# Performance work log

Hardware: AMD Instinct MI355X
Metric: run time of the kernel (lower is better)

## Reference

```python
import jax, jax.numpy as jnp
import numpy as np

DIM = 768
NUM_HEADS = 12
HEAD_DIM = DIM // NUM_HEADS
HW = 32  # input_size = (32, 32)


def setup_inputs() -> dict:
    key = jax.random.key(0)
    ks = jax.random.split(key, 7)
    return {
        "x": jax.random.normal(ks[0], (8, HW, HW, DIM), dtype=jnp.float32),
        "w_qkv": jax.random.normal(ks[1], (DIM, 3 * DIM), dtype=jnp.float32) * 0.02,
        "b_qkv": jnp.zeros((3 * DIM,), dtype=jnp.float32),
        "w_proj": jax.random.normal(ks[2], (DIM, DIM), dtype=jnp.float32) * 0.02,
        "b_proj": jnp.zeros((DIM,), dtype=jnp.float32),
        "rel_pos_h": jax.random.normal(ks[3], (2 * HW - 1, HEAD_DIM), dtype=jnp.float32) * 0.02,
        "rel_pos_w": jax.random.normal(ks[4], (2 * HW - 1, HEAD_DIM), dtype=jnp.float32) * 0.02,
    }


def _gather_rel_pos(size, rel_pos):
    # q_size == k_size == size, so no resize; index = i - j + (size - 1)
    idx = jnp.arange(size)[:, None] - jnp.arange(size)[None, :] + (size - 1)
    return rel_pos[idx]  # [size, size, head_dim]


def reference(x, w_qkv, b_qkv, w_proj, b_proj, rel_pos_h, rel_pos_w):
    B, H, W, C = x.shape
    nH, D = NUM_HEADS, HEAD_DIM
    scale = D ** -0.5
    S = H * W

    qkv = x.reshape(B, S, C) @ w_qkv + b_qkv          # [B,S,3C]
    qkv = qkv.reshape(B, S, 3, nH, D).transpose(2, 0, 3, 1, 4)  # [3,B,nH,S,D]
    q, k, v = qkv[0], qkv[1], qkv[2]

    attn = jnp.einsum('bnsd,bntd->bnst', q * scale, k)  # [B,nH,S,S]

    # decomposed relative positional bias
    Rh = _gather_rel_pos(H, rel_pos_h)                  # [H,H,D]
    Rw = _gather_rel_pos(W, rel_pos_w)                  # [W,W,D]
    r_q = q.reshape(B, nH, H, W, D)
    rel_h = jnp.einsum('bnhwc,hkc->bnhwk', r_q, Rh)     # [B,nH,H,W,H]
    rel_w = jnp.einsum('bnhwc,wkc->bnhwk', r_q, Rw)     # [B,nH,H,W,W]
    attn = (attn.reshape(B, nH, H, W, H, W)
            + rel_h[..., :, None]
            + rel_w[..., None, :]).reshape(B, nH, S, S)

    attn = jax.nn.softmax(attn, axis=-1)
    out = jnp.einsum('bnst,bntd->bnsd', attn, v)        # [B,nH,S,D]
    out = out.transpose(0, 2, 1, 3).reshape(B, H, W, C)
    return out @ w_proj + b_proj
```

## Files before the change

kernel.cpp:

```cpp
#include <hip/hip_runtime.h>
#include <cstdint>
#include <cstddef>

#define NH 12
#define HDIM 64
#define C_ 768
#define C3 2304
#define SEQ 1024
#define LS 72
#define LSV 76
#define SMAX 6.0f
#define LOG2E 1.4426950408889634f

typedef short bf16x8_t __attribute__((ext_vector_type(8)));
typedef float f32x4_t __attribute__((ext_vector_type(4)));
typedef unsigned short u16x4_t __attribute__((ext_vector_type(4)));

__device__ __forceinline__ unsigned short bf16_rne(float x) {
    unsigned int u = __float_as_uint(x);
    u += 0x7FFFu + ((u >> 16) & 1u);
    return (unsigned short)(u >> 16);
}
__device__ __forceinline__ float bf16f(unsigned short h) {
    return __uint_as_float(((unsigned int)h) << 16);
}

__device__ __forceinline__ void load_lds16(const unsigned short* g, unsigned short* l) {
    auto gp = (const __attribute__((address_space(1))) unsigned short*)(uintptr_t)g;
    auto lp = (__attribute__((address_space(3))) unsigned short*)(uint32_t)(uintptr_t)l;
    __builtin_amdgcn_global_load_lds(gp, lp, 16, 0, 0);
}

__device__ __forceinline__ int swz(int row, int g) {
    const int pr = row >> 1;
    const int ch = (((row & 1) << 2) | g) ^ (pr & 7);
    return pr * 64 + ch * 8;
}

__device__ __forceinline__ void splitT_body(const float* __restrict__ W,
                                            unsigned short* __restrict__ Thi,
                                            unsigned short* __restrict__ Tlo,
                                            int Kdim, int Ndim, int kb, int nb,
                                            float (*tile)[33], int t)
{
    const int lr = t >> 3, lc = (t & 7) * 4;
    *(float4*)&tile[lr][lc] = *(const float4*)&W[(size_t)(kb + lr) * Ndim + nb + lc];
    __syncthreads();
    const float v0 = tile[lc + 0][lr];
    const float v1 = tile[lc + 1][lr];
    const float v2 = tile[lc + 2][lr];
    const float v3 = tile[lc + 3][lr];
    u16x4_t h, l;
    h.x = bf16_rne(v0); l.x = bf16_rne(v0 - bf16f(h.x));
    h.y = bf16_rne(v1); l.y = bf16_rne(v1 - bf16f(h.y));
    h.z = bf16_rne(v2); l.z = bf16_rne(v2 - bf16f(h.z));
    h.w = bf16_rne(v3); l.w = bf16_rne(v3 - bf16f(h.w));
    *(u16x4_t*)&Thi[(size_t)(nb + lr) * Kdim + kb + lc] = h;
    *(u16x4_t*)&Tlo[(size_t)(nb + lr) * Kdim + kb + lc] = l;
}

__global__ __launch_bounds__(256)
void prep_kernel(const float* __restrict__ x, const float* __restrict__ w_qkv,
                 const float* __restrict__ w_proj,
                 const float* __restrict__ rel_h, const float* __restrict__ rel_w,
                 unsigned short* __restrict__ xhi,
                 unsigned short* __restrict__ wqh, unsigned short* __restrict__ wql,
                 unsigned short* __restrict__ wph, unsigned short* __restrict__ wpl,
                 unsigned short* __restrict__ relcat)
{
    __shared__ float tile[32][33];
    const int bid = blockIdx.x, tid = threadIdx.x;
    if (bid < 6144) {
        const int i = bid * 256 + tid;
        float4 v = ((const float4*)x)[i];
        u16x4_t h;
        h.x = bf16_rne(v.x); h.y = bf16_rne(v.y); h.z = bf16_rne(v.z); h.w = bf16_rne(v.w);
        ((u16x4_t*)xhi)[i] = h;
    } else if (bid < 7872) {
        const int local = bid - 6144;
        const int bx = local % 72, by = local / 72;
        splitT_body(w_qkv, wqh, wql, C_, C3, by * 32, bx * 32, tile, tid);
    } else if (bid < 8448) {
        const int local = bid - 7872;
        const int bx = local % 24, by = local / 24;
        splitT_body(w_proj, wph, wpl, C_, C_, by * 32, bx * 32, tile, tid);
    } else {
        const int i = (bid - 8448) * 256 + tid;
        if (i < 2016) {
            const int j = i * 4;
            const int row = j >> 6, col = j & 63;
            const float* src = row < 63 ? &rel_h[row * 64 + col] : &rel_w[(row - 63) * 64 + col];
            const float4 v = *(const float4*)src;
            u16x4_t h;
            h.x = bf16_rne(v.x); h.y = bf16_rne(v.y); h.z = bf16_rne(v.z); h.w = bf16_rne(v.w);
            *(u16x4_t*)&relcat[j] = h;
        }
    }
}

__global__ __launch_bounds__(256, 4)
void qkvgemm_kernel(const unsigned short* __restrict__ Ahi, const unsigned short* __restrict__ BThi,
                    const float* __restrict__ bias,
                    unsigned short* __restrict__ q_hi, unsigned short* __restrict__ k_hi,
                    unsigned short* __restrict__ vT)
{
    constexpr int K = 768;
    __shared__ unsigned short As[2][4096];
    __shared__ unsigned short Bs[2][4096];
    const int tid = threadIdx.x;
    const int w = tid >> 6, lane = tid & 63, g = lane >> 4, r = lane & 15;
    const int wr = (w >> 1) * 64, wc = (w & 1) * 64;

    const int bid  = blockIdx.x;
    const int xcd  = bid & 7;
    const int idx  = bid >> 3;
    const int msub = idx & 7;
    const int ntile = idx >> 3;
    const int m0 = (xcd * 8 + msub) * 128;
    const int n0 = ntile * 128;

    int row_[2], gc_[2];
#pragma unroll
    for (int i = 0; i < 2; ++i) {
        const int s = i * 256 + tid;
        const int pr = s >> 3;
        const int u = (s & 7) ^ (pr & 7);
        row_[i] = pr * 2 + (u >> 2);
        gc_[i]  = u & 3;
    }
    const unsigned short* gA0 = Ahi + (size_t)(m0 + row_[0]) * K + gc_[0] * 8;
    const unsigned short* gA1 = Ahi + (size_t)(m0 + row_[1]) * K + gc_[1] * 8;
    const unsigned short* gB0 = BThi + (size_t)(n0 + row_[0]) * K + gc_[0] * 8;
    const unsigned short* gB1 = BThi + (size_t)(n0 + row_[1]) * K + gc_[1] * 8;
    const int lofs0 = w * 512;
    const int lofs1 = 2048 + w * 512;

    f32x4_t acc[4][4];
#pragma unroll
    for (int i = 0; i < 4; ++i)
#pragma unroll
        for (int j = 0; j < 4; ++j)
#pragma unroll
            for (int q = 0; q < 4; ++q) acc[i][j][q] = 0.f;

    load_lds16(gA0, &As[0][lofs0]);
    load_lds16(gA1, &As[0][lofs1]);
    load_lds16(gB0, &Bs[0][lofs0]);
    load_lds16(gB1, &Bs[0][lofs1]);

    int cur = 0;
    for (int k0 = 0; k0 < K; k0 += 32) {
        __syncthreads();
        if (k0 + 32 < K) {
            const int nb2 = cur ^ 1;
            load_lds16(gA0 + k0 + 32, &As[nb2][lofs0]);
            load_lds16(gA1 + k0 + 32, &As[nb2][lofs1]);
            load_lds16(gB0 + k0 + 32, &Bs[nb2][lofs0]);
            load_lds16(gB1 + k0 + 32, &Bs[nb2][lofs1]);
        }
        bf16x8_t am[4];
#pragma unroll
        for (int i = 0; i < 4; ++i)
            am[i] = *(const bf16x8_t*)&As[cur][swz(wr + 16 * i + r, g)];
        __builtin_amdgcn_s_setprio(1);
#pragma unroll
        for (int j = 0; j < 4; ++j) {
            const bf16x8_t bn = *(const bf16x8_t*)&Bs[cur][swz(wc + 16 * j + r, g)];
#pragma unroll
            for (int i = 0; i < 4; ++i)
                acc[i][j] = __builtin_amdgcn_mfma_f32_16x16x32_bf16(am[i], bn, acc[i][j], 0, 0, 0);
        }
        __builtin_amdgcn_s_setprio(0);
        cur ^= 1;
    }

    const int third = n0 >= 1536 ? 2 : (n0 >= 768 ? 1 : 0);
    if (third == 2) {
#pragma unroll
        for (int j = 0; j < 4; ++j) {
            const int n = n0 + wc + 16 * j + r;
            const float bj = bias[n];
            const int nn = n - 1536;
            const int h = nn >> 6, d = nn & 63;
#pragma unroll
            for (int i = 0; i < 4; ++i) {
                const int m = m0 + wr + 16 * i + 4 * g;
                const int b = m >> 10, t = m & 1023;
                const size_t hb = ((size_t)(b * NH + h)) << 16;
                u16x4_t pv;
#pragma unroll
                for (int q = 0; q < 4; ++q)
                    pv[q] = bf16_rne(acc[i][j][q] + bj);
                *(u16x4_t*)&vT[hb + (size_t)d * 1024 + t] = pv;
            }
        }
    } else {
        unsigned short* outH = third == 1 ? k_hi : q_hi;
#pragma unroll
        for (int j = 0; j < 4; ++j) {
            const int n = n0 + wc + 16 * j + r;
            const float bj = bias[n];
            const int nn = n - third * 768;
            const int h = nn >> 6, d = nn & 63;
#pragma unroll
            for (int i = 0; i < 4; ++i) {
                const int m = m0 + wr + 16 * i + 4 * g;
                const int b = m >> 10, t = m & 1023;
                const size_t hb = ((size_t)(b * NH + h)) << 16;
                unsigned short* dh = outH + hb + (size_t)t * 64 + d;
#pragma unroll
                for (int q = 0; q < 4; ++q)
                    dh[(size_t)q * 64] = bf16_rne(acc[i][j][q] + bj);
            }
        }
    }
}

__global__ __launch_bounds__(256, 2)
void projgemm_kernel(const unsigned short* __restrict__ Ahi, const unsigned short* __restrict__ Alo,
                     const unsigned short* __restrict__ BThi, const unsigned short* __restrict__ BTlo,
                     const float* __restrict__ bias, float* __restrict__ C)
{
    constexpr int K = 768;
    constexpr int N = C_;
    __shared__ unsigned short Ash[2][4096], Asl[2][4096];
    __shared__ unsigned short Bsh[2][4096], Bsl[2][4096];
    const int tid = threadIdx.x;
    const int w = tid >> 6, lane = tid & 63, g = lane >> 4, r = lane & 15;
    const int wr = (w >> 1) * 64, wc = (w & 1) * 64;

    const int bid  = blockIdx.x;
    const int xcd  = bid & 7;
    const int idx  = bid >> 3;
    const int msub = idx & 7;
    const int ntile = idx >> 3;
    const int m0 = (xcd * 8 + msub) * 128;
    const int n0 = ntile * 128;

    int row_[2], gc_[2];
#pragma unroll
    for (int i = 0; i < 2; ++i) {
        const int s = i * 256 + tid;
        const int pr = s >> 3;
        const int u = (s & 7) ^ (pr & 7);
        row_[i] = pr * 2 + (u >> 2);
        gc_[i]  = u & 3;
    }
    const unsigned short* gAh0 = Ahi + (size_t)(m0 + row_[0]) * K + gc_[0] * 8;
    const unsigned short* gAh1 = Ahi + (size_t)(m0 + row_[1]) * K + gc_[1] * 8;
    const unsigned short* gAl0 = Alo + (size_t)(m0 + row_[0]) * K + gc_[0] * 8;
    const unsigned short* gAl1 = Alo + (size_t)(m0 + row_[1]) * K + gc_[1] * 8;
    const unsigned short* gBh0 = BThi + (size_t)(n0 + row_[0]) * K + gc_[0] * 8;
    const unsigned short* gBh1 = BThi + (size_t)(n0 + row_[1]) * K + gc_[1] * 8;
    const unsigned short* gBl0 = BTlo + (size_t)(n0 + row_[0]) * K + gc_[0] * 8;
    const unsigned short* gBl1 = BTlo + (size_t)(n0 + row_[1]) * K + gc_[1] * 8;
    const int lofs0 = w * 512;
    const int lofs1 = 2048 + w * 512;

    f32x4_t acc[4][4];
#pragma unroll
    for (int i = 0; i < 4; ++i)
#pragma unroll
        for (int j = 0; j < 4; ++j)
#pragma unroll
            for (int q = 0; q < 4; ++q) acc[i][j][q] = 0.f;

    load_lds16(gAh0, &Ash[0][lofs0]);
    load_lds16(gAh1, &Ash[0][lofs1]);
    load_lds16(gAl0, &Asl[0][lofs0]);
    load_lds16(gAl1, &Asl[0][lofs1]);
    load_lds16(gBh0, &Bsh[0][lofs0]);
    load_lds16(gBh1, &Bsh[0][lofs1]);
    load_lds16(gBl0, &Bsl[0][lofs0]);
    load_lds16(gBl1, &Bsl[0][lofs1]);

    int cur = 0;
    for (int k0 = 0; k0 < K; k0 += 32) {
        __syncthreads();
        if (k0 + 32 < K) {
            const int nb2 = cur ^ 1;
            load_lds16(gAh0 + k0 + 32, &Ash[nb2][lofs0]);
            load_lds16(gAh1 + k0 + 32, &Ash[nb2][lofs1]);
            load_lds16(gAl0 + k0 + 32, &Asl[nb2][lofs0]);
            load_lds16(gAl1 + k0 + 32, &Asl[nb2][lofs1]);
            load_lds16(gBh0 + k0 + 32, &Bsh[nb2][lofs0]);
            load_lds16(gBh1 + k0 + 32, &Bsh[nb2][lofs1]);
            load_lds16(gBl0 + k0 + 32, &Bsl[nb2][lofs0]);
            load_lds16(gBl1 + k0 + 32, &Bsl[nb2][lofs1]);
        }
        bf16x8_t amh[4], aml[4];
#pragma unroll
        for (int i = 0; i < 4; ++i) {
            const int o = swz(wr + 16 * i + r, g);
            amh[i] = *(const bf16x8_t*)&Ash[cur][o];
            aml[i] = *(const bf16x8_t*)&Asl[cur][o];
        }
        __builtin_amdgcn_s_setprio(1);
#pragma unroll
        for (int j = 0; j < 4; ++j) {
            const int o = swz(wc + 16 * j + r, g);
            const bf16x8_t bnh = *(const bf16x8_t*)&Bsh[cur][o];
            const bf16x8_t bnl = *(const bf16x8_t*)&Bsl[cur][o];
#pragma unroll
            for (int i = 0; i < 4; ++i) {
                acc[i][j] = __builtin_amdgcn_mfma_f32_16x16x32_bf16(amh[i], bnh, acc[i][j], 0, 0, 0);
                acc[i][j] = __builtin_amdgcn_mfma_f32_16x16x32_bf16(amh[i], bnl, acc[i][j], 0, 0, 0);
                acc[i][j] = __builtin_amdgcn_mfma_f32_16x16x32_bf16(aml[i], bnh, acc[i][j], 0, 0, 0);
            }
        }
        __builtin_amdgcn_s_setprio(0);
        cur ^= 1;
    }

#pragma unroll
    for (int j = 0; j < 4; ++j) {
        const float bj = bias[n0 + wc + 16 * j + r];
#pragma unroll
        for (int i = 0; i < 4; ++i) {
            float* Cp = C + (size_t)(m0 + wr + 16 * i + 4 * g) * N + n0 + wc + 16 * j + r;
#pragma unroll
            for (int q = 0; q < 4; ++q)
                Cp[(size_t)q * N] = acc[i][j][q] + bj;
        }
    }
}

__global__ __launch_bounds__(256, 4)
void relgemm_kernel(const unsigned short* __restrict__ qhi, const unsigned short* __restrict__ relcat,
                    unsigned short* __restrict__ G)
{
    __shared__ unsigned short bs[128 * LS];
    const int tid = threadIdx.x;
    const int sb = blockIdx.x, bh = blockIdx.y;
    const int w = tid >> 6, lane = tid & 63, g = lane >> 4, r = lane & 15;
    const size_t hb = (size_t)bh << 16;

    {
        const int row = tid >> 1, c32 = (tid & 1) * 32;
        if (row < 126) {
#pragma unroll
            for (int e = 0; e < 4; ++e)
                *(bf16x8_t*)&bs[row * LS + c32 + 8 * e] =
                    *(const bf16x8_t*)&relcat[row * 64 + c32 + 8 * e];
        } else {
            const bf16x8_t z = {0,0,0,0,0,0,0,0};
#pragma unroll
            for (int e = 0; e < 4; ++e)
                *(bf16x8_t*)&bs[row * LS + c32 + 8 * e] = z;
        }
    }
    bf16x8_t aq[2][2];
#pragma unroll
    for (int i = 0; i < 2; ++i)
#pragma unroll
        for (int c = 0; c < 2; ++c)
            aq[i][c] = *(const bf16x8_t*)(qhi + hb + (size_t)(sb * 128 + w * 32 + 16 * i + r) * 64 + c * 32 + 8 * g);
    __syncthreads();

    f32x4_t acc[2][8];
#pragma unroll
    for (int i = 0; i < 2; ++i)
#pragma unroll
        for (int fj = 0; fj < 8; ++fj)
#pragma unroll
            for (int q = 0; q < 4; ++q) acc[i][fj][q] = 0.f;

#pragma unroll
    for (int c = 0; c < 2; ++c)
#pragma unroll
        for (int fj = 0; fj < 8; ++fj) {
            const bf16x8_t brel = *(const bf16x8_t*)&bs[(16 * fj + r) * LS + c * 32 + 8 * g];
#pragma unroll
            for (int i = 0; i < 2; ++i)
                acc[i][fj] = __builtin_amdgcn_mfma_f32_16x16x32_bf16(aq[i][c], brel, acc[i][fj], 0, 0, 0);
        }

    unsigned short* Gb = G + (((size_t)bh << 10) + sb * 128 + w * 32) * 128;
#pragma unroll
    for (int i = 0; i < 2; ++i)
#pragma unroll
        for (int reg = 0; reg < 4; ++reg) {
            unsigned short* Gr = Gb + (size_t)(16 * i + 4 * g + reg) * 128 + r;
#pragma unroll
            for (int fj = 0; fj < 8; ++fj)
                Gr[16 * fj] = bf16_rne(acc[i][fj][reg]);
        }
}

__global__ __launch_bounds__(256, 4)
void attn12_kernel(const unsigned short* __restrict__ qhi,
                   const unsigned short* __restrict__ khi,
                   const unsigned short* __restrict__ vT,
                   const unsigned short* __restrict__ G,
                   unsigned short* __restrict__ outh, unsigned short* __restrict__ outl)
{
    __shared__ unsigned short ksh[2 * 64 * LS];
    __shared__ unsigned short vsh[2 * 64 * LSV];

    const int tid  = threadIdx.x;
    const int bh   = blockIdx.x;
    const int s0   = blockIdx.y * 64;
    const int w    = tid >> 6;
    const int lane = tid & 63;
    const int g    = lane >> 4;
    const int r    = lane & 15;
    const size_t hb = (size_t)bh << 16;

    bf16x8_t aq[2];
#pragma unroll
    for (int c = 0; c < 2; ++c)
        aq[c] = *(const bf16x8_t*)(qhi + hb + (size_t)(s0 + w * 16 + r) * 64 + c * 32 + 8 * g);

    const unsigned short* Gbh = G + ((size_t)bh << 17);
    const int q    = s0 + w * 16 + r;
    const int qoff = q * 128;
    const int qcb  = (q >> 5) + 31;
    const int iw   = q & 31;
    float bw[4][2];
#pragma unroll
    for (int reg = 0; reg < 4; ++reg)
#pragma unroll
        for (int jh = 0; jh < 2; ++jh)
            bw[reg][jh] = bf16f(Gbh[qoff + 94 + iw - 16 * jh - 4 * g - reg]) * LOG2E;

    f32x4_t oacc[4];
    float lsum[4];
#pragma unroll
    for (int i = 0; i < 4; ++i) {
        lsum[i] = 0.f;
#pragma unroll
        for (int j = 0; j < 4; ++j) oacc[i][j] = 0.f;
    }

    const int krow = tid >> 2, kc16 = (tid & 3) * 16;
    const int vd = tid >> 3, vt = (tid & 7) * 8;
    const int addr_a = (((g & 1) << 5) + r) << 2;
    const int addr_b = addr_a + 64;
    const bool lowg = g < 2;

    {
        const unsigned short* kh = khi + hb + (size_t)krow * 64 + kc16;
        const bf16x8_t a0 = *(const bf16x8_t*)kh;
        const bf16x8_t a1 = *(const bf16x8_t*)(kh + 8);
        const bf16x8_t va = *(const bf16x8_t*)(vT + hb + (size_t)vd * 1024 + vt);
        const bf16x8_t vb = *(const bf16x8_t*)(vT + hb + (size_t)(vd + 32) * 1024 + vt);
        *(bf16x8_t*)&ksh[krow * LS + kc16]     = a0;
        *(bf16x8_t*)&ksh[krow * LS + kc16 + 8] = a1;
        *(bf16x8_t*)&vsh[vd * LSV + vt]        = va;
        *(bf16x8_t*)&vsh[(vd + 32) * LSV + vt] = vb;
    }
    __syncthreads();

    int cur = 0;
    for (int t0 = 0; t0 < SEQ; t0 += 64) {
        const int cok = cur * 64 * LS;
        const int cov = cur * 64 * LSV;
        const int tn = (t0 + 64 < SEQ) ? t0 + 64 : t0;
        bf16x8_t nk0, nk1, nva, nvb;
        {
            const unsigned short* kh = khi + hb + (size_t)(tn + krow) * 64 + kc16;
            nk0 = *(const bf16x8_t*)kh;
            nk1 = *(const bf16x8_t*)(kh + 8);
            nva = *(const bf16x8_t*)(vT + hb + (size_t)vd * 1024 + tn + vt);
            nvb = *(const bf16x8_t*)(vT + hb + (size_t)(vd + 32) * 1024 + tn + vt);
        }

        f32x4_t sacc[4];
#pragma unroll
        for (int fj = 0; fj < 4; ++fj)
#pragma unroll
            for (int j = 0; j < 4; ++j) sacc[fj][j] = 0.f;
#pragma unroll
        for (int c = 0; c < 2; ++c)
#pragma unroll
            for (int fj = 0; fj < 4; ++fj) {
                const bf16x8_t bkh = *(const bf16x8_t*)&ksh[cok + (16 * fj + r) * LS + c * 32 + 8 * g];
                sacc[fj] = __builtin_amdgcn_mfma_f32_16x16x32_bf16(bkh, aq[c], sacc[fj], 0, 0, 0);
            }

        const int kh0 = t0 >> 5;
        const float bh0 = (bf16f(Gbh[qoff + qcb - kh0])     - SMAX) * LOG2E;
        const float bh1 = (bf16f(Gbh[qoff + qcb - kh0 - 1]) - SMAX) * LOG2E;
#pragma unroll
        for (int fj = 0; fj < 4; ++fj)
#pragma unroll
            for (int reg = 0; reg < 4; ++reg) {
                const float s = fmaf(sacc[fj][reg], 0.125f * LOG2E,
                                     ((fj >> 1) ? bh1 : bh0) + bw[reg][fj & 1]);
                const float e = exp2f(s);
                sacc[fj][reg] = e;
                lsum[reg] += e;
            }

        unsigned int pk01[4], pk23[4];
#pragma unroll
        for (int fj = 0; fj < 4; ++fj) {
            asm("v_cvt_pk_bf16_f32 %0, %1, %2" : "=v"(pk01[fj]) : "v"(sacc[fj][0]), "v"(sacc[fj][1]));
            asm("v_cvt_pk_bf16_f32 %0, %1, %2" : "=v"(pk23[fj]) : "v"(sacc[fj][2]), "v"(sacc[fj][3]));
        }

#pragma unroll
        for (int c = 0; c < 2; ++c) {
            const int a01A = __builtin_amdgcn_ds_bpermute(addr_a, (int)pk01[2 * c]);
            const int a23A = __builtin_amdgcn_ds_bpermute(addr_a, (int)pk23[2 * c]);
            const int b01A = __builtin_amdgcn_ds_bpermute(addr_b, (int)pk01[2 * c]);
            const int b23A = __builtin_amdgcn_ds_bpermute(addr_b, (int)pk23[2 * c]);
            const int a01B = __builtin_amdgcn_ds_bpermute(addr_a, (int)pk01[2 * c + 1]);
            const int a23B = __builtin_amdgcn_ds_bpermute(addr_a, (int)pk23[2 * c + 1]);
            const int b01B = __builtin_amdgcn_ds_bpermute(addr_b, (int)pk01[2 * c + 1]);
            const int b23B = __builtin_amdgcn_ds_bpermute(addr_b, (int)pk23[2 * c + 1]);
            union { int u[4]; bf16x8_t v; } pf;
            pf.u[0] = lowg ? a01A : a01B;
            pf.u[1] = lowg ? a23A : a23B;
            pf.u[2] = lowg ? b01A : b01B;
            pf.u[3] = lowg ? b23A : b23B;
#pragma unroll
            for (int fd = 0; fd < 4; ++fd) {
                const bf16x8_t bvh = *(const bf16x8_t*)&vsh[cov + (16 * fd + r) * LSV + c * 32 + 8 * g];
                oacc[fd] = __builtin_amdgcn_mfma_f32_16x16x32_bf16(bvh, pf.v, oacc[fd], 0, 0, 0);
            }
        }

        const int nok = (cur ^ 1) * 64 * LS;
        const int nov = (cur ^ 1) * 64 * LSV;
        *(bf16x8_t*)&ksh[nok + krow * LS + kc16]      = nk0;
        *(bf16x8_t*)&ksh[nok + krow * LS + kc16 + 8]  = nk1;
        *(bf16x8_t*)&vsh[nov + vd * LSV + vt]         = nva;
        *(bf16x8_t*)&vsh[nov + (vd + 32) * LSV + vt]  = nvb;
        __syncthreads();
        cur ^= 1;
    }

    const int b = bh / NH, h = bh - (bh / NH) * NH;
    float rs = (lsum[0] + lsum[1]) + (lsum[2] + lsum[3]);
    rs += __shfl_xor(rs, 16);
    rs += __shfl_xor(rs, 32);
    const float rinv = 1.f / rs;
    unsigned short* oph = outh + ((size_t)b * SEQ + q) * C_ + h * HDIM + 4 * g;
    unsigned short* opl = outl + ((size_t)b * SEQ + q) * C_ + h * HDIM + 4 * g;
#pragma unroll
    for (int fd = 0; fd < 4; ++fd) {
        u16x4_t hv, lv;
#pragma unroll
        for (int reg = 0; reg < 4; ++reg) {
            const float v = oacc[fd][reg] * rinv;
            const unsigned short hh = bf16_rne(v);
            hv[reg] = hh;
            lv[reg] = bf16_rne(v - bf16f(hh));
        }
        *(u16x4_t*)(oph + 16 * fd) = hv;
        *(u16x4_t*)(opl + 16 * fd) = lv;
    }
}

extern "C" void kernel_launch(void* const* d_in, const int* in_sizes, int n_in,
                              void* d_out, int out_size, void* d_ws, size_t ws_size,
                              hipStream_t stream) {
    (void)in_sizes; (void)n_in; (void)out_size; (void)ws_size;
    const float* x      = (const float*)d_in[0];
    const float* w_qkv  = (const float*)d_in[1];
    const float* b_qkv  = (const float*)d_in[2];
    const float* w_proj = (const float*)d_in[3];
    const float* b_proj = (const float*)d_in[4];
    const float* rel_h  = (const float*)d_in[5];
    const float* rel_w  = (const float*)d_in[6];
    float* out = (float*)d_out;

    char* base = (char*)d_ws;
    unsigned short* xhi    = (unsigned short*)(base + 0);
    unsigned short* xlo    = (unsigned short*)(base + 12582912);
    unsigned short* wqh    = (unsigned short*)(base + 25165824);
    unsigned short* wql    = (unsigned short*)(base + 28704768);
    unsigned short* wph    = (unsigned short*)(base + 32243712);
    unsigned short* wpl    = (unsigned short*)(base + 33423360);
    unsigned short* qhi    = (unsigned short*)(base + 34603008);
    unsigned short* relcat = (unsigned short*)(base + 47185920);
    unsigned short* khi    = (unsigned short*)(base + 59768832);
    unsigned short* vT     = (unsigned short*)(base + 84934656);
    unsigned short* G      = (unsigned short*)(base + 110100480);
    unsigned short* ohif   = xhi;
    unsigned short* olo    = xlo;

    prep_kernel<<<8456, 256, 0, stream>>>(x, w_qkv, w_proj, rel_h, rel_w,
                                          xhi, wqh, wql, wph, wpl, relcat);
    qkvgemm_kernel<<<1152, 256, 0, stream>>>(xhi, wqh, b_qkv, qhi, khi, vT);
    {
        dim3 grid(8, 96);
        relgemm_kernel<<<grid, 256, 0, stream>>>(qhi, relcat, G);
    }
    {
        dim3 grid(96, SEQ / 64);
        attn12_kernel<<<grid, 256, 0, stream>>>(qhi, khi, vT, G, ohif, olo);
    }
    projgemm_kernel<<<384, 256, 0, stream>>>(ohif, olo, wph, wpl, b_proj, out);
}
```

Baseline: 162.2 us.

## Load K and V fragments directly from global memory, dropping LDS staging

The attention kernel no longer stages K and V tiles through double-buffered shared memory with block-wide barriers. Each wave now reads its MFMA operand fragments straight from global memory (relying on L1/L2 caching, since the four waves share the same K/V tiles). This removes the LDS writes, LDS reads and per-iteration __syncthreads, but each wave now issues redundant global loads, and the V fragment reads are strided across rows, which may raise cache traffic and latency.

```diff
diff --git a/kernel.cpp b/kernel.cpp
--- a/kernel.cpp
+++ b/kernel.cpp
@@ -8,7 +8,6 @@
 #define C3 2304
 #define SEQ 1024
 #define LS 72
-#define LSV 76
 #define SMAX 6.0f
 #define LOG2E 1.4426950408889634f
 
@@ -388,15 +387,12 @@
 }
 
 __global__ __launch_bounds__(256, 4)
-void attn12_kernel(const unsigned short* __restrict__ qhi,
+void attn13_kernel(const unsigned short* __restrict__ qhi,
                    const unsigned short* __restrict__ khi,
                    const unsigned short* __restrict__ vT,
                    const unsigned short* __restrict__ G,
                    unsigned short* __restrict__ outh, unsigned short* __restrict__ outl)
 {
-    __shared__ unsigned short ksh[2 * 64 * LS];
-    __shared__ unsigned short vsh[2 * 64 * LSV];
-
     const int tid  = threadIdx.x;
     const int bh   = blockIdx.x;
     const int s0   = blockIdx.y * 64;
@@ -432,39 +428,14 @@
         for (int j = 0; j < 4; ++j) oacc[i][j] = 0.f;
     }
 
-    const int krow = tid >> 2, kc16 = (tid & 3) * 16;
-    const int vd = tid >> 3, vt = (tid & 7) * 8;
+    const unsigned short* Kb = khi + hb + (size_t)r * 64 + 8 * g;
+    const unsigned short* Vb = vT + hb + (size_t)r * 1024 + 8 * g;
+
     const int addr_a = (((g & 1) << 5) + r) << 2;
     const int addr_b = addr_a + 64;
     const bool lowg = g < 2;
 
-    {
-        const unsigned short* kh = khi + hb + (size_t)krow * 64 + kc16;
-        const bf16x8_t a0 = *(const bf16x8_t*)kh;
-        const bf16x8_t a1 = *(const bf16x8_t*)(kh + 8);
-        const bf16x8_t va = *(const bf16x8_t*)(vT + hb + (size_t)vd * 1024 + vt);
-        const bf16x8_t vb = *(const bf16x8_t*)(vT + hb + (size_t)(vd + 32) * 1024 + vt);
-        *(bf16x8_t*)&ksh[krow * LS + kc16]     = a0;
-        *(bf16x8_t*)&ksh[krow * LS + kc16 + 8] = a1;
-        *(bf16x8_t*)&vsh[vd * LSV + vt]        = va;
-        *(bf16x8_t*)&vsh[(vd + 32) * LSV + vt] = vb;
-    }
-    __syncthreads();
-
-    int cur = 0;
     for (int t0 = 0; t0 < SEQ; t0 += 64) {
-        const int cok = cur * 64 * LS;
-        const int cov = cur * 64 * LSV;
-        const int tn = (t0 + 64 < SEQ) ? t0 + 64 : t0;
-        bf16x8_t nk0, nk1, nva, nvb;
-        {
-            const unsigned short* kh = khi + hb + (size_t)(tn + krow) * 64 + kc16;
-            nk0 = *(const bf16x8_t*)kh;
-            nk1 = *(const bf16x8_t*)(kh + 8);
-            nva = *(const bf16x8_t*)(vT + hb + (size_t)vd * 1024 + tn + vt);
-            nvb = *(const bf16x8_t*)(vT + hb + (size_t)(vd + 32) * 1024 + tn + vt);
-        }
-
         f32x4_t sacc[4];
 #pragma unroll
         for (int fj = 0; fj < 4; ++fj)
@@ -474,9 +445,16 @@
         for (int c = 0; c < 2; ++c)
 #pragma unroll
             for (int fj = 0; fj < 4; ++fj) {
-                const bf16x8_t bkh = *(const bf16x8_t*)&ksh[cok + (16 * fj + r) * LS + c * 32 + 8 * g];
+                const bf16x8_t bkh = *(const bf16x8_t*)(Kb + (size_t)(t0 + 16 * fj) * 64 + c * 32);
                 sacc[fj] = __builtin_amdgcn_mfma_f32_16x16x32_bf16(bkh, aq[c], sacc[fj], 0, 0, 0);
             }
+
+        bf16x8_t bv[2][4];
+#pragma unroll
+        for (int c = 0; c < 2; ++c)
+#pragma unroll
+            for (int fd = 0; fd < 4; ++fd)
+                bv[c][fd] = *(const bf16x8_t*)(Vb + (size_t)fd * 16384 + t0 + 32 * c);
 
         const int kh0 = t0 >> 5;
         const float bh0 = (bf16f(Gbh[qoff + qcb - kh0])     - SMAX) * LOG2E;
@@ -515,20 +493,9 @@
             pf.u[2] = lowg ? b01A : b01B;
             pf.u[3] = lowg ? b23A : b23B;
 #pragma unroll
-            for (int fd = 0; fd < 4; ++fd) {
-                const bf16x8_t bvh = *(const bf16x8_t*)&vsh[cov + (16 * fd + r) * LSV + c * 32 + 8 * g];
-                oacc[fd] = __builtin_amdgcn_mfma_f32_16x16x32_bf16(bvh, pf.v, oacc[fd], 0, 0, 0);
-            }
-        }
-
-        const int nok = (cur ^ 1) * 64 * LS;
-        const int nov = (cur ^ 1) * 64 * LSV;
-        *(bf16x8_t*)&ksh[nok + krow * LS + kc16]      = nk0;
-        *(bf16x8_t*)&ksh[nok + krow * LS + kc16 + 8]  = nk1;
-        *(bf16x8_t*)&vsh[nov + vd * LSV + vt]         = nva;
-        *(bf16x8_t*)&vsh[nov + (vd + 32) * LSV + vt]  = nvb;
-        __syncthreads();
-        cur ^= 1;
+            for (int fd = 0; fd < 4; ++fd)
+                oacc[fd] = __builtin_amdgcn_mfma_f32_16x16x32_bf16(bv[c][fd], pf.v, oacc[fd], 0, 0, 0);
+        }
     }
 
     const int b = bh / NH, h = bh - (bh / NH) * NH;
@@ -590,7 +557,7 @@
     }
     {
         dim3 grid(96, SEQ / 64);
-        attn12_kernel<<<grid, 256, 0, stream>>>(qhi, khi, vT, G, ohif, olo);
+        attn13_kernel<<<grid, 256, 0, stream>>>(qhi, khi, vT, G, ohif, olo);
     }
     projgemm_kernel<<<384, 256, 0, stream>>>(ohif, olo, wph, wpl, b_proj, out);
 }
```

New measurement: 279.6 us. +72.4%, slower.
